# Performance work log

Measured on AMD Instinct MI355X. Metric: run time of the kernel, lower is better.

The kernel has to match this reference:

```python
import jax, jax.numpy as jnp
import numpy as np

H = 8          # num_channels (heads)
POS = 16       # pos_dim
MAX_F = 16.0
MIN_F = 1.0
HALF_S = 16    # samples_per_dim=32 -> offsets -16..16, S=33
SCALE = POS ** -0.5


def setup_inputs() -> dict:
    key = jax.random.key(0)
    ks = jax.random.split(key, 12)
    B, L, C = 2, 4096, 1024
    p = 0.02
    return {
        'x': jax.random.normal(ks[0], (B, L, C), jnp.float32),
        'wave_w': jax.random.normal(ks[1], (C, 3 * H), jnp.float32) * p,
        'wave_b': jax.random.normal(ks[2], (3 * H,), jnp.float32) * p,
        'query_w': jax.random.normal(ks[3], (C, H * POS), jnp.float32) * p,
        'query_b': jax.random.normal(ks[4], (H * POS,), jnp.float32) * p,
        'key_w': jax.random.normal(ks[5], (POS,), jnp.float32) * p,
        'out_w': jax.random.normal(ks[6], (C, C), jnp.float32) * p,
        'se1_w': jax.random.normal(ks[7], (C, C // 4), jnp.float32) * p,
        'se1_b': jax.random.normal(ks[8], (C // 4,), jnp.float32) * p,
        'se2_w': jax.random.normal(ks[9], (C // 4, C), jnp.float32) * p,
        'se2_b': jax.random.normal(ks[10], (C,), jnp.float32) * p,
    }


def _adaptive_conv(x, wave_w, wave_b, query_w, query_b, key_w, out_w,
                   se1_w, se1_b, se2_w, se2_b):
    B, L, C = x.shape
    D = C // H
    silu = jax.nn.silu
    offsets = jnp.arange(-HALF_S, HALF_S + 1, dtype=x.dtype)  # [S]
    S = offsets.shape[0]

    # wave params -> freq/phase/decay per (B,L,H)
    wave = silu(x @ wave_w + wave_b).reshape(B, L, 3, H)
    freq = jax.nn.sigmoid(wave[:, :, 0, :]) * (MAX_F - MIN_F) + MIN_F
    phase = jnp.tanh(wave[:, :, 1, :]) * MAX_F
    decay = jax.nn.sigmoid(wave[:, :, 2, :]) * 9.5 + 0.5
    queries = silu(x @ query_w + query_b).reshape(B, L, H, POS)

    freq_avg = freq.mean(axis=-1)    # [B,L]
    phase_avg = phase.mean(axis=-1)  # [B,L]

    centers = jnp.arange(L, dtype=x.dtype)
    # [B,L,S] real-valued sample positions
    sample_pos = (centers[None, :, None]
                  + offsets[None, None, :] * freq_avg[..., None]
                  + phase_avg[..., None])
    valid = (sample_pos >= 0) & (sample_pos < L)           # [B,L,S]
    sample_idx = jnp.clip(sample_pos.astype(jnp.int32), 0, L - 1)

    # gather: values[b,l,s,:] = x[b, sample_idx[b,l,s], :]
    values = jnp.take_along_axis(x, sample_idx.reshape(B, L * S, 1), axis=1)
    values = values.reshape(B, L, S, H, D).transpose(0, 1, 3, 2, 4)  # [B,L,H,S,D]

    rel = jnp.abs(offsets)[None, None, None, :] * freq[..., None]    # [B,L,H,S]
    keys = silu(rel[..., None] * key_w)                              # [B,L,H,S,POS]
    logits = jnp.einsum('blhd,blhsd->blhs', queries, keys) * SCALE

    vmask = valid[:, :, None, :]                                     # [B,L,H,S]
    logits = jnp.where(vmask, logits, -1e30)
    env = jnp.exp(-rel / jnp.maximum(decay[..., None], 0.1))
    w = jax.nn.softmax(logits, axis=-1) * env * vmask.astype(x.dtype)
    w = w / (w.sum(axis=-1, keepdims=True) + 1e-8)

    out = jnp.einsum('blhsd,blhs->blhd', values, w).reshape(B, L, C)
    se = jax.nn.sigmoid(silu(out @ se1_w + se1_b) @ se2_w + se2_b)
    out = out * se
    return silu(out @ out_w)


def reference(x, wave_w, wave_b, query_w, query_b, key_w, out_w,
              se1_w, se1_b, se2_w, se2_b):
    return _adaptive_conv(x, wave_w, wave_b, query_w, query_b, key_w,
                          out_w, se1_w, se1_b, se2_w, se2_b)
```

## Files before the change

### kernel.cpp

```cpp
#include <hip/hip_runtime.h>
#include <math.h>

#define HN 8
#define POSN 16
#define SN 33
#define HALF_SN 16
#define CDIM 1024
#define LDIM 4096
#define BDIM 2
#define NTOK (BDIM * LDIM)

typedef unsigned short u16;
typedef short short8 __attribute__((ext_vector_type(8)));
typedef u16 u16x8 __attribute__((ext_vector_type(8)));
typedef unsigned int u32x4 __attribute__((ext_vector_type(4)));
typedef float f32x4 __attribute__((ext_vector_type(4)));

__device__ __forceinline__ float sigf(float x) { return 1.0f / (1.0f + expf(-x)); }
__device__ __forceinline__ float siluf(float x) { return x / (1.0f + expf(-x)); }
__device__ __forceinline__ float frcp(float x) { return __builtin_amdgcn_rcpf(x); }
__device__ __forceinline__ float fexp(float x) { return __expf(x); }
__device__ __forceinline__ float fsig(float x) { return frcp(1.0f + fexp(-x)); }
__device__ __forceinline__ float fsilu(float x) { return x * fsig(x); }

__device__ __forceinline__ u16 f2b(float f) {
    union { float f; unsigned u; } v; v.f = f;
    unsigned r = v.u + 0x7fffu + ((v.u >> 16) & 1u);
    return (u16)(r >> 16);
}
__device__ __forceinline__ float b2f(u16 v) {
    union { unsigned u; float f; } x; x.u = ((unsigned)v) << 16; return x.f;
}
__device__ __forceinline__ float u2f(unsigned u) {
    union { unsigned u; float f; } x; x.u = u; return x.f;
}
__device__ __forceinline__ void ld_lds16(const void* g, void* l) {
    __builtin_amdgcn_global_load_lds(
        (const __attribute__((address_space(1))) void*)g,
        (__attribute__((address_space(3))) void*)l, 16, 0, 0);
}

__global__ __launch_bounds__(256) void transcast_all(
    const float* __restrict__ qw, const float* __restrict__ s1,
    const float* __restrict__ s2, const float* __restrict__ ow,
    const float* __restrict__ ww,
    u16* __restrict__ oq, u16* __restrict__ o1,
    u16* __restrict__ o2, u16* __restrict__ oo,
    float* __restrict__ owT)
{
    const int bid = blockIdx.x;
    if (bid >= 1664) {
        const int idx = (bid - 1664) * 256 + threadIdx.x;
        const int c = idx >> 10, k = idx & 1023;
        owT[idx] = ww[k * 24 + c];
        return;
    }
    const float* in; u16* out; int N, K, base;
    if      (bid < 128) { in = qw; out = oq; N = 128;  K = 1024; base = 0;   }
    else if (bid < 384) { in = s1; out = o1; N = 256;  K = 1024; base = 128; }
    else if (bid < 640) { in = s2; out = o2; N = 1024; K = 256;  base = 384; }
    else                { in = ow; out = oo; N = 1024; K = 1024; base = 640; }
    const int rel = bid - base, nx = N / 32;
    const int bn = (rel % nx) * 32, bk = (rel / nx) * 32;

    __shared__ float tile[32][33];
    const int tx = threadIdx.x & 31, ty = threadIdx.x >> 5;
    #pragma unroll
    for (int yy = ty; yy < 32; yy += 8)
        tile[yy][tx] = in[(size_t)(bk + yy) * N + bn + tx];
    __syncthreads();
    #pragma unroll
    for (int yy = ty; yy < 32; yy += 8)
        out[(size_t)(bn + yy) * K + bk + tx] = f2b(tile[tx][yy]);
}

__global__ __launch_bounds__(256) void wave_partial(
    const float* __restrict__ x, const float* __restrict__ wwT,
    u16* __restrict__ xbf, float* __restrict__ part)
{
    const int bid = blockIdx.x;
    const int sl = bid >> 7;
    const int tg = bid & 127;
    const int tid = threadIdx.x;
    const int t0 = tg * 64;
    const int k0 = sl * 128;

    __shared__ float wsct[24][128];

    for (int i = tid; i < 768; i += 256) {
        const int c = i >> 5, k4 = (i & 31) * 4;
        *(float4*)&wsct[c][k4] = *(const float4*)(wwT + (size_t)c * 1024 + k0 + k4);
    }
    for (int i = tid; i < 1024; i += 256) {
        const int r = i >> 4, c8 = (i & 15) * 8;
        const float* src = x + (size_t)(t0 + r) * CDIM + k0 + c8;
        float4 a = *(const float4*)(src);
        float4 b = *(const float4*)(src + 4);
        u16x8 o;
        o[0]=f2b(a.x); o[1]=f2b(a.y); o[2]=f2b(a.z); o[3]=f2b(a.w);
        o[4]=f2b(b.x); o[5]=f2b(b.y); o[6]=f2b(b.z); o[7]=f2b(b.w);
        *(u16x8*)(xbf + (size_t)(t0 + r) * CDIM + k0 + c8) = o;
    }
    __syncthreads();

    const int tok = tid & 63;
    const int cg  = tid >> 6;
    const int t = t0 + tok;
    const float* xr = x + (size_t)t * CDIM + k0;
    const int c0 = cg * 6;
    float a0=0.f, a1=0.f, a2=0.f, a3=0.f, a4=0.f, a5=0.f;

    #pragma unroll 4
    for (int kk = 0; kk < 128; kk += 4) {
        float4 xv = *(const float4*)(xr + kk);
        float4 w0 = *(const float4*)&wsct[c0 + 0][kk];
        float4 w1 = *(const float4*)&wsct[c0 + 1][kk];
        float4 w2 = *(const float4*)&wsct[c0 + 2][kk];
        float4 w3 = *(const float4*)&wsct[c0 + 3][kk];
        float4 w4 = *(const float4*)&wsct[c0 + 4][kk];
        float4 w5 = *(const float4*)&wsct[c0 + 5][kk];
        a0 += xv.x*w0.x; a0 += xv.y*w0.y; a0 += xv.z*w0.z; a0 += xv.w*w0.w;
        a1 += xv.x*w1.x; a1 += xv.y*w1.y; a1 += xv.z*w1.z; a1 += xv.w*w1.w;
        a2 += xv.x*w2.x; a2 += xv.y*w2.y; a2 += xv.z*w2.z; a2 += xv.w*w2.w;
        a3 += xv.x*w3.x; a3 += xv.y*w3.y; a3 += xv.z*w3.z; a3 += xv.w*w3.w;
        a4 += xv.x*w4.x; a4 += xv.y*w4.y; a4 += xv.z*w4.z; a4 += xv.w*w4.w;
        a5 += xv.x*w5.x; a5 += xv.y*w5.y; a5 += xv.z*w5.z; a5 += xv.w*w5.w;
    }
    float* pp = part + (size_t)sl * NTOK * 24 + (size_t)t * 24 + c0;
    pp[0]=a0; pp[1]=a1; pp[2]=a2; pp[3]=a3; pp[4]=a4; pp[5]=a5;
}

template <int MODE, int CFG>
__global__ __launch_bounds__(256) void mfma_gemm(
    const u16* __restrict__ A, const u16* __restrict__ Bt,
    const float* __restrict__ bias, const u16* __restrict__ mulb,
    void* __restrict__ Cptr, int M, int N, int K)
{
    constexpr int BM  = (CFG == 0) ? 128 : 64;
    constexpr int MI  = (CFG == 0) ? 4 : 2;
    constexpr int NJ  = 4;
    constexpr int ACH = BM / 16;
    constexpr int NCH = ACH + 8;

    __shared__ u16 lds[2][(BM + 128) * 32];

    const int nwg = gridDim.x * gridDim.y;
    const int flat = blockIdx.y * gridDim.x + blockIdx.x;
    const int swz = (flat & 7) * (nwg >> 3) + (flat >> 3);
    const int bxi = swz / gridDim.y, byi = swz % gridDim.y;

    const int tid = threadIdx.x;
    const int bm = bxi * BM, bn = byi * 128;
    const int wid = tid >> 6, lane = tid & 63;
    const int wr = (CFG == 0) ? (wid >> 1) * 64 : (wid >> 1) * 32;
    const int wc = (wid & 1) * 64;
    const int fm = lane & 15;
    const int kg = (lane >> 4) * 8;
    const int lrow = lane >> 2;
    const int lk   = (lane & 3) * 8;

    f32x4 acc[MI][NJ];
    #pragma unroll
    for (int i = 0; i < MI; ++i)
        #pragma unroll
        for (int j = 0; j < NJ; ++j) acc[i][j] = (f32x4){0.f, 0.f, 0.f, 0.f};

    auto stage = [&](u16* dst, int k0s) {
        #pragma unroll
        for (int c = wid; c < NCH; c += 4) {
            const u16* gsrc = (c < ACH)
                ? A  + (size_t)(bm + c * 16 + lrow) * K + k0s + lk
                : Bt + (size_t)(bn + (c - ACH) * 16 + lrow) * K + k0s + lk;
            ld_lds16(gsrc, dst + c * 512 + lane * 8);
        }
    };

    stage(&lds[0][0], 0);
    __syncthreads();
    int cur = 0;
    for (int k0 = 0; k0 < K; k0 += 32) {
        const int k1 = (k0 + 32 < K) ? (k0 + 32) : k0;
        stage(&lds[cur ^ 1][0], k1);
        short8 a[MI], b[NJ];
        #pragma unroll
        for (int i = 0; i < MI; ++i)
            a[i] = *(const short8*)&lds[cur][(wr + i * 16 + fm) * 32 + kg];
        #pragma unroll
        for (int j = 0; j < NJ; ++j)
            b[j] = *(const short8*)&lds[cur][(BM + wc + j * 16 + fm) * 32 + kg];
        #pragma unroll
        for (int i = 0; i < MI; ++i)
            #pragma unroll
            for (int j = 0; j < NJ; ++j)
                acc[i][j] = __builtin_amdgcn_mfma_f32_16x16x32_bf16(a[i], b[j], acc[i][j], 0, 0, 0);
        __syncthreads();
        cur ^= 1;
    }

    float* Cf = (float*)Cptr;
    u16* Cb = (u16*)Cptr;
    #pragma unroll
    for (int i = 0; i < MI; ++i) {
        const int row0 = bm + wr + i * 16 + (lane >> 4) * 4;
        #pragma unroll
        for (int j = 0; j < NJ; ++j) {
            const int col = bn + wc + j * 16 + fm;
            const float vb = (MODE == 3) ? 0.0f : bias[col];
            #pragma unroll
            for (int e = 0; e < 4; ++e) {
                const int row = row0 + e;
                float v = acc[i][j][e];
                if (MODE == 1) v = fsilu(v + vb);
                if (MODE == 2) v = fsig(v + vb) * b2f(mulb[(size_t)row * N + col]);
                if (MODE == 3) v = fsilu(v);
                if (MODE == 3) Cf[(size_t)row * N + col] = v;
                else           Cb[(size_t)row * N + col] = f2b(v);
            }
        }
    }
}

__global__ __launch_bounds__(256) void adaptconv_kernel(
    const u16* __restrict__ xbf, const float* __restrict__ key_w,
    const u16* __restrict__ qb, const float* __restrict__ part,
    const float* __restrict__ wave_b, u16* __restrict__ out)
{
    const int bid = blockIdx.x;
    const int swz = (bid & 7) * (NTOK / 16) + (bid >> 3);
    const int sub = threadIdx.x >> 7, lt = threadIdx.x & 127;
    const int t = swz * 2 + sub;
    const int b = t / LDIM, l = t % LDIM;
    const int h = lt >> 4;
    const int li = lt & 15;

    __shared__ float qs[2][HN][17];
    __shared__ float kw[POSN];
    __shared__ float wpre[2][24];
    __shared__ float psh_s[2][HN];
    __shared__ float favg_s[2], pavg_s[2];
    __shared__ float fr[2][HN], dc[2][HN];
    __shared__ int   boff[2][SN];
    __shared__ float msk[2][SN];
    __shared__ float vsh[2][HN][17];
    __shared__ float esh[2][HN][17];
    __shared__ float wgt[2][HN][SN];

    qs[sub][lt >> 4][lt & 15] = b2f(qb[(size_t)t * 128 + lt]);
    if (threadIdx.x < POSN) kw[threadIdx.x] = key_w[threadIdx.x];

    if (lt < 24) {
        float s = wave_b[lt];
        #pragma unroll
        for (int sl = 0; sl < 8; ++sl)
            s += part[(size_t)sl * NTOK * 24 + (size_t)t * 24 + lt];
        wpre[sub][lt] = siluf(s);
    }
    __syncthreads();
    if (lt < HN) {
        float f = sigf(wpre[sub][lt])      * 15.0f + 1.0f;
        float p = tanhf(wpre[sub][8 + lt]) * 16.0f;
        float d = sigf(wpre[sub][16 + lt]) * 9.5f + 0.5f;
        fr[sub][lt] = f; dc[sub][lt] = d; psh_s[sub][lt] = p;
    }
    __syncthreads();
    if (lt == 0) {
        float fa = 0.f, pa = 0.f;
        for (int hh = 0; hh < HN; ++hh) { fa += fr[sub][hh]; pa += psh_s[sub][hh]; }
        favg_s[sub] = fa * 0.125f; pavg_s[sub] = pa * 0.125f;
    }
    __syncthreads();
    if (lt < SN) {
        float fa = favg_s[sub], pa = pavg_s[sub];
        float sp = (float)l + (float)(lt - HALF_SN) * fa + pa;
        bool v = (sp >= 0.0f) && (sp < (float)LDIM);
        int si = (int)sp;
        si = min(max(si, 0), LDIM - 1);
        boff[sub][lt] = si * (CDIM * 2);
        msk[sub][lt] = v ? 1.0f : 0.0f;
    }
    __syncthreads();

    {
        const float fh = fr[sub][h];
        const float rdci = frcp(fmaxf(dc[sub][h], 0.1f));
        for (int ds = li; ds < 17; ds += 16) {
            float rel = (float)ds * fh;
            float acc = 0.0f;
            #pragma unroll
            for (int p = 0; p < POSN; ++p)
                acc += qs[sub][h][p] * fsilu(rel * kw[p]);
            vsh[sub][h][ds] = 0.25f * acc;
            esh[sub][h][ds] = fexp(-rel * rdci);
        }
    }
    __syncthreads();

    {
        const int ns = (li == 0) ? 3 : 2;
        int   sI[3] = { li, li + 16, 32 };
        float lg[3];
        #pragma unroll
        for (int k = 0; k < 3; ++k) {
            if (k < ns) {
                const int s = sI[k], ds = abs(s - 16);
                lg[k] = (msk[sub][s] != 0.0f) ? vsh[sub][h][ds] : -1e30f;
            } else lg[k] = -3.4e38f;
        }
        float m = fmaxf(lg[0], fmaxf(lg[1], lg[2]));
        #pragma unroll
        for (int d = 1; d < 16; d <<= 1) m = fmaxf(m, __shfl_xor(m, d));

        float e[3]; float ssum = 0.0f;
        #pragma unroll
        for (int k = 0; k < 3; ++k) {
            e[k] = (k < ns) ? fexp(lg[k] - m) : 0.0f;
            ssum += e[k];
        }
        #pragma unroll
        for (int d = 1; d < 16; d <<= 1) ssum += __shfl_xor(ssum, d);

        const float rss = frcp(ssum);
        float wv[3]; float wsum = 0.0f;
        #pragma unroll
        for (int k = 0; k < 3; ++k) {
            if (k < ns) {
                const int s = sI[k], ds = abs(s - 16);
                wv[k] = e[k] * rss * esh[sub][h][ds] * msk[sub][s];
            } else wv[k] = 0.0f;
            wsum += wv[k];
        }
        #pragma unroll
        for (int d = 1; d < 16; d <<= 1) wsum += __shfl_xor(wsum, d);

        const float inv = frcp(wsum + 1e-8f);
        #pragma unroll
        for (int k = 0; k < 3; ++k)
            if (k < ns) wgt[sub][h][sI[k]] = wv[k] * inv;
    }
    __syncthreads();

    const char* xbB = (const char*)(xbf + (size_t)b * LDIM * CDIM);
    const int cbyte = lt * 16;
    float a0=0,a1=0,a2=0,a3=0,a4=0,a5=0,a6=0,a7=0;

    #define GFMA(V, W) do { \
        a0 += (W) * u2f((V)[0] << 16); a1 += (W) * u2f((V)[0] & 0xffff0000u); \
        a2 += (W) * u2f((V)[1] << 16); a3 += (W) * u2f((V)[1] & 0xffff0000u); \
        a4 += (W) * u2f((V)[2] << 16); a5 += (W) * u2f((V)[2] & 0xffff0000u); \
        a6 += (W) * u2f((V)[3] << 16); a7 += (W) * u2f((V)[3] & 0xffff0000u); } while (0)

    int s = 0;
    for (; s + 4 <= SN; s += 4) {
        u32x4 v0 = *(const u32x4*)(xbB + boff[sub][s]     + cbyte);
        u32x4 v1 = *(const u32x4*)(xbB + boff[sub][s + 1] + cbyte);
        u32x4 v2 = *(const u32x4*)(xbB + boff[sub][s + 2] + cbyte);
        u32x4 v3 = *(const u32x4*)(xbB + boff[sub][s + 3] + cbyte);
        float w0 = wgt[sub][h][s],     w1 = wgt[sub][h][s + 1];
        float w2 = wgt[sub][h][s + 2], w3 = wgt[sub][h][s + 3];
        GFMA(v0, w0); GFMA(v1, w1); GFMA(v2, w2); GFMA(v3, w3);
    }
    for (; s < SN; ++s) {
        u32x4 v = *(const u32x4*)(xbB + boff[sub][s] + cbyte);
        float w = wgt[sub][h][s];
        GFMA(v, w);
    }
    #undef GFMA

    u16x8 o;
    o[0]=f2b(a0); o[1]=f2b(a1); o[2]=f2b(a2); o[3]=f2b(a3);
    o[4]=f2b(a4); o[5]=f2b(a5); o[6]=f2b(a6); o[7]=f2b(a7);
    *(u16x8*)(out + (size_t)t * CDIM + lt * 8) = o;
}

extern "C" void kernel_launch(void* const* d_in, const int* in_sizes, int n_in,
                              void* d_out, int out_size, void* d_ws, size_t ws_size,
                              hipStream_t stream)
{
    const float* x       = (const float*)d_in[0];
    const float* wave_w  = (const float*)d_in[1];
    const float* wave_b  = (const float*)d_in[2];
    const float* query_w = (const float*)d_in[3];
    const float* query_b = (const float*)d_in[4];
    const float* key_w   = (const float*)d_in[5];
    const float* out_w   = (const float*)d_in[6];
    const float* se1_w   = (const float*)d_in[7];
    const float* se1_b   = (const float*)d_in[8];
    const float* se2_w   = (const float*)d_in[9];
    const float* se2_b   = (const float*)d_in[10];

    char* wsb = (char*)d_ws;
    u16* q_bf    = (u16*)wsb;           wsb += (size_t)NTOK * 128 * 2;
    u16* x_bf    = (u16*)wsb;           wsb += (size_t)NTOK * CDIM * 2;
    u16* conv_bf = (u16*)wsb;           wsb += (size_t)NTOK * CDIM * 2;
    u16* tmp1_bf = (u16*)wsb;           wsb += (size_t)NTOK * 256 * 2;
    u16* g_bf    = (u16*)wsb;           wsb += (size_t)NTOK * CDIM * 2;
    u16* qw_bf   = (u16*)wsb;           wsb += (size_t)128 * CDIM * 2;
    u16* se1w_bf = (u16*)wsb;           wsb += (size_t)256 * CDIM * 2;
    u16* se2w_bf = (u16*)wsb;           wsb += (size_t)CDIM * 256 * 2;
    u16* outw_bf = (u16*)wsb;           wsb += (size_t)CDIM * CDIM * 2;
    float* wwT   = (float*)wsb;         wsb += (size_t)24 * CDIM * 4;
    float* part  = (float*)wsb;         wsb += (size_t)8 * NTOK * 24 * 4;

    transcast_all<<<1760, 256, 0, stream>>>(
        query_w, se1_w, se2_w, out_w, wave_w,
        qw_bf, se1w_bf, se2w_bf, outw_bf, wwT);

    wave_partial<<<8 * 128, 256, 0, stream>>>(x, wwT, x_bf, part);

    mfma_gemm<1, 2><<<dim3(NTOK / 64, 1), 256, 0, stream>>>(
        x_bf, qw_bf, query_b, nullptr, q_bf, NTOK, 128, CDIM);

    adaptconv_kernel<<<NTOK / 2, 256, 0, stream>>>(
        x_bf, key_w, q_bf, part, wave_b, conv_bf);

    mfma_gemm<1, 2><<<dim3(NTOK / 64, 256 / 128), 256, 0, stream>>>(
        conv_bf, se1w_bf, se1_b, nullptr, tmp1_bf, NTOK, 256, CDIM);

    mfma_gemm<2, 0><<<dim3(NTOK / 128, CDIM / 128), 256, 0, stream>>>(
        tmp1_bf, se2w_bf, se2_b, conv_bf, g_bf, NTOK, CDIM, 256);

    mfma_gemm<3, 0><<<dim3(NTOK / 128, CDIM / 128), 256, 0, stream>>>(
        g_bf, outw_bf, nullptr, nullptr, d_out, NTOK, CDIM, CDIM);
}
```

Baseline: 134.7 us.

## Merge weight transcast and wave partial kernels; pack gather FMAs into float2

Merges the weight transpose/cast kernel and the wave-projection partial kernel into one launch. The wave weights are now transposed on the fly into shared memory instead of going through a separate wwT buffer. This removes one launch and one intermediate round trip through global memory. Separately, the gather accumulation in the adaptive conv kernel now uses float2 vectors, which may let the compiler emit packed FMA instructions. The cost is more block-level branching in the merged kernel and strided scalar writes to shared memory.

```diff
diff --git a/kernel.cpp b/kernel.cpp
--- a/kernel.cpp
+++ b/kernel.cpp
@@ -15,6 +15,7 @@
 typedef u16 u16x8 __attribute__((ext_vector_type(8)));
 typedef unsigned int u32x4 __attribute__((ext_vector_type(4)));
 typedef float f32x4 __attribute__((ext_vector_type(4)));
+typedef float f32x2 __attribute__((ext_vector_type(2)));
 
 __device__ __forceinline__ float sigf(float x) { return 1.0f / (1.0f + expf(-x)); }
 __device__ __forceinline__ float siluf(float x) { return x / (1.0f + expf(-x)); }
@@ -40,56 +41,55 @@
         (__attribute__((address_space(3))) void*)l, 16, 0, 0);
 }
 
-__global__ __launch_bounds__(256) void transcast_all(
+__global__ __launch_bounds__(256) void prep_kernel(
     const float* __restrict__ qw, const float* __restrict__ s1,
     const float* __restrict__ s2, const float* __restrict__ ow,
-    const float* __restrict__ ww,
+    const float* __restrict__ ww, const float* __restrict__ x,
     u16* __restrict__ oq, u16* __restrict__ o1,
     u16* __restrict__ o2, u16* __restrict__ oo,
-    float* __restrict__ owT)
-{
-    const int bid = blockIdx.x;
-    if (bid >= 1664) {
-        const int idx = (bid - 1664) * 256 + threadIdx.x;
-        const int c = idx >> 10, k = idx & 1023;
-        owT[idx] = ww[k * 24 + c];
-        return;
-    }
-    const float* in; u16* out; int N, K, base;
-    if      (bid < 128) { in = qw; out = oq; N = 128;  K = 1024; base = 0;   }
-    else if (bid < 384) { in = s1; out = o1; N = 256;  K = 1024; base = 128; }
-    else if (bid < 640) { in = s2; out = o2; N = 1024; K = 256;  base = 384; }
-    else                { in = ow; out = oo; N = 1024; K = 1024; base = 640; }
-    const int rel = bid - base, nx = N / 32;
-    const int bn = (rel % nx) * 32, bk = (rel / nx) * 32;
-
-    __shared__ float tile[32][33];
-    const int tx = threadIdx.x & 31, ty = threadIdx.x >> 5;
-    #pragma unroll
-    for (int yy = ty; yy < 32; yy += 8)
-        tile[yy][tx] = in[(size_t)(bk + yy) * N + bn + tx];
-    __syncthreads();
-    #pragma unroll
-    for (int yy = ty; yy < 32; yy += 8)
-        out[(size_t)(bn + yy) * K + bk + tx] = f2b(tile[tx][yy]);
-}
-
-__global__ __launch_bounds__(256) void wave_partial(
-    const float* __restrict__ x, const float* __restrict__ wwT,
     u16* __restrict__ xbf, float* __restrict__ part)
 {
     const int bid = blockIdx.x;
-    const int sl = bid >> 7;
-    const int tg = bid & 127;
     const int tid = threadIdx.x;
+
+    if (bid < 1664) {
+        const float* in; u16* out; int N, K, base;
+        if      (bid < 128) { in = qw; out = oq; N = 128;  K = 1024; base = 0;   }
+        else if (bid < 384) { in = s1; out = o1; N = 256;  K = 1024; base = 128; }
+        else if (bid < 640) { in = s2; out = o2; N = 1024; K = 256;  base = 384; }
+        else                { in = ow; out = oo; N = 1024; K = 1024; base = 640; }
+        const int rel = bid - base, nx = N / 32;
+        const int bn = (rel % nx) * 32, bk = (rel / nx) * 32;
+
+        __shared__ float tile[32][33];
+        const int tx = tid & 31, ty = tid >> 5;
+        #pragma unroll
+        for (int yy = ty; yy < 32; yy += 8)
+            tile[yy][tx] = in[(size_t)(bk + yy) * N + bn + tx];
+        __syncthreads();
+        #pragma unroll
+        for (int yy = ty; yy < 32; yy += 8)
+            out[(size_t)(bn + yy) * K + bk + tx] = f2b(tile[tx][yy]);
+        return;
+    }
+
+    const int pid = bid - 1664;
+    const int sl = pid >> 7;
+    const int tg = pid & 127;
     const int t0 = tg * 64;
     const int k0 = sl * 128;
 
     __shared__ float wsct[24][128];
 
-    for (int i = tid; i < 768; i += 256) {
-        const int c = i >> 5, k4 = (i & 31) * 4;
-        *(float4*)&wsct[c][k4] = *(const float4*)(wwT + (size_t)c * 1024 + k0 + k4);
+    {
+        const float* wsrc = ww + (size_t)k0 * 24;
+        for (int i = tid; i < 768; i += 256) {
+            float4 v = *(const float4*)(wsrc + i * 4);
+            const int p = i * 4;
+            const int k = p / 24, c0 = p % 24;
+            wsct[c0 + 0][k] = v.x; wsct[c0 + 1][k] = v.y;
+            wsct[c0 + 2][k] = v.z; wsct[c0 + 3][k] = v.w;
+        }
     }
     for (int i = tid; i < 1024; i += 256) {
         const int r = i >> 4, c8 = (i & 15) * 8;
@@ -341,13 +341,15 @@
 
     const char* xbB = (const char*)(xbf + (size_t)b * LDIM * CDIM);
     const int cbyte = lt * 16;
-    float a0=0,a1=0,a2=0,a3=0,a4=0,a5=0,a6=0,a7=0;
+    f32x2 ac0 = {0.f, 0.f}, ac1 = {0.f, 0.f}, ac2 = {0.f, 0.f}, ac3 = {0.f, 0.f};
 
     #define GFMA(V, W) do { \
-        a0 += (W) * u2f((V)[0] << 16); a1 += (W) * u2f((V)[0] & 0xffff0000u); \
-        a2 += (W) * u2f((V)[1] << 16); a3 += (W) * u2f((V)[1] & 0xffff0000u); \
-        a4 += (W) * u2f((V)[2] << 16); a5 += (W) * u2f((V)[2] & 0xffff0000u); \
-        a6 += (W) * u2f((V)[3] << 16); a7 += (W) * u2f((V)[3] & 0xffff0000u); } while (0)
+        f32x2 ww_ = { (W), (W) }; \
+        f32x2 p0 = { u2f((V)[0] << 16), u2f((V)[0] & 0xffff0000u) }; \
+        f32x2 p1 = { u2f((V)[1] << 16), u2f((V)[1] & 0xffff0000u) }; \
+        f32x2 p2 = { u2f((V)[2] << 16), u2f((V)[2] & 0xffff0000u) }; \
+        f32x2 p3 = { u2f((V)[3] << 16), u2f((V)[3] & 0xffff0000u) }; \
+        ac0 += ww_ * p0; ac1 += ww_ * p1; ac2 += ww_ * p2; ac3 += ww_ * p3; } while (0)
 
     int s = 0;
     for (; s + 4 <= SN; s += 4) {
@@ -367,8 +369,8 @@
     #undef GFMA
 
     u16x8 o;
-    o[0]=f2b(a0); o[1]=f2b(a1); o[2]=f2b(a2); o[3]=f2b(a3);
-    o[4]=f2b(a4); o[5]=f2b(a5); o[6]=f2b(a6); o[7]=f2b(a7);
+    o[0]=f2b(ac0[0]); o[1]=f2b(ac0[1]); o[2]=f2b(ac1[0]); o[3]=f2b(ac1[1]);
+    o[4]=f2b(ac2[0]); o[5]=f2b(ac2[1]); o[6]=f2b(ac3[0]); o[7]=f2b(ac3[1]);
     *(u16x8*)(out + (size_t)t * CDIM + lt * 8) = o;
 }
 
@@ -398,14 +400,11 @@
     u16* se1w_bf = (u16*)wsb;           wsb += (size_t)256 * CDIM * 2;
     u16* se2w_bf = (u16*)wsb;           wsb += (size_t)CDIM * 256 * 2;
     u16* outw_bf = (u16*)wsb;           wsb += (size_t)CDIM * CDIM * 2;
-    float* wwT   = (float*)wsb;         wsb += (size_t)24 * CDIM * 4;
     float* part  = (float*)wsb;         wsb += (size_t)8 * NTOK * 24 * 4;
 
-    transcast_all<<<1760, 256, 0, stream>>>(
-        query_w, se1_w, se2_w, out_w, wave_w,
-        qw_bf, se1w_bf, se2w_bf, outw_bf, wwT);
-
-    wave_partial<<<8 * 128, 256, 0, stream>>>(x, wwT, x_bf, part);
+    prep_kernel<<<2688, 256, 0, stream>>>(
+        query_w, se1_w, se2_w, out_w, wave_w, x,
+        qw_bf, se1w_bf, se2w_bf, outw_bf, x_bf, part);
 
     mfma_gemm<1, 2><<<dim3(NTOK / 64, 1), 256, 0, stream>>>(
         x_bf, qw_bf, query_b, nullptr, q_bf, NTOK, 128, CDIM);
```

Result: slower. 144.3 us (+7.1%).
